# Optimization experiments

Hardware: AMD Instinct MI355X
Metric: run time of the kernel (lower is better)

## Reference

```python
import jax, jax.numpy as jnp
import numpy as np


def _prelu(x, a):
    return jnp.where(x >= 0, x, a * x)


def _conv1x1(x, w, b, a):
    # x: [N,C,H,W], w: [O,C], b: [O] -> PReLU(conv1x1(x))
    y = jnp.einsum('oc,nchw->nohw', w, x) + b[None, :, None, None]
    return _prelu(y, a)


def setup_inputs() -> dict:
    key = jax.random.key(0)
    ks = jax.random.split(key, 8)
    N, C, H, W = 4, 128, 64, 64
    Cr = C // 2  # reduction=2
    sC = 1.0 / np.sqrt(C)
    x = jax.random.normal(ks[0], (N, C, H, W), dtype=jnp.float32)
    w1 = jax.random.normal(ks[1], (Cr, C), dtype=jnp.float32) * sC
    b1 = jnp.zeros((Cr,), dtype=jnp.float32)
    a1 = jnp.asarray(0.25, dtype=jnp.float32)  # PReLU (single shared slope)
    w2 = jax.random.normal(ks[2], (Cr, C), dtype=jnp.float32) * sC
    b2 = jnp.zeros((Cr,), dtype=jnp.float32)
    a2 = jnp.asarray(0.25, dtype=jnp.float32)
    wa = jax.random.normal(ks[3], (C, C), dtype=jnp.float32) * sC
    ba = jnp.zeros((C,), dtype=jnp.float32)
    aa = jnp.asarray(0.25, dtype=jnp.float32)
    return {"x": x, "w1": w1, "b1": b1, "a1": a1,
            "w2": w2, "b2": b2, "a2": a2,
            "wa": wa, "ba": ba, "aa": aa}


def reference(x, w1, b1, a1, w2, b2, a2, wa, ba, aa):
    N, C, H, W = x.shape
    HW = H * W
    e1 = _conv1x1(x, w1, b1, a1).reshape(N, -1, HW)   # [N,Cr,HW]
    e2 = _conv1x1(x, w2, b2, a2).reshape(N, -1, HW)   # [N,Cr,HW]
    asm = _conv1x1(x, wa, ba, aa).reshape(N, C, HW)   # [N,C,HW]
    # ksize=1: per-channel outer products summed over channels == single contraction
    score = jnp.einsum('nci,ncj->nij', e1, e2)        # [N,HW,HW]
    score = jax.nn.softmax(score, axis=2)
    out = jnp.einsum('nij,ncj->nci', score, asm)      # [N,C,HW]
    return out.reshape(N, C, H, W)
```

## Files before the change

### kernel.cpp

```cpp
#include <hip/hip_runtime.h>
#include <hip/hip_bf16.h>
#include <stdint.h>


typedef float   f32x16 __attribute__((ext_vector_type(16)));
typedef __bf16  bf16x8 __attribute__((ext_vector_type(8)));
typedef __bf16  bf16x2 __attribute__((ext_vector_type(2)));
typedef unsigned int u32x4 __attribute__((ext_vector_type(4)));
typedef unsigned int u32x2 __attribute__((ext_vector_type(2)));

#define L2E 1.4426950408889634f
#define NSHIFT (-12.0f * L2E)

#define Q_OFF   (0u)
#define K_OFF   (2u << 20)
#define V_OFF   (4u << 20)
#define DEN_OFF (8u << 20)
#define XTH_OFF ((8u << 20) + (1u << 19))
#define XTL_OFF (XTH_OFF + (4u << 20))
#define WH_OFF  (XTL_OFF + (4u << 20))
#define WL_OFF  (WH_OFF + (1u << 16))
#define OP_OFF  XTH_OFF

__device__ inline unsigned short f2bf(float f) {
  unsigned u = __builtin_bit_cast(unsigned, f);
  return (unsigned short)((u + 0x7FFFu + ((u >> 16) & 1u)) >> 16);
}
__device__ inline float bf2f(unsigned short h) {
  unsigned u = ((unsigned)h) << 16;
  return __builtin_bit_cast(float, u);
}

__device__ inline void gld_lds16(const void* g, void* l) {
  __builtin_amdgcn_global_load_lds(
      (const __attribute__((address_space(1))) unsigned*)g,
      (__attribute__((address_space(3))) unsigned*)l, 16, 0, 0);
}

__global__ __launch_bounds__(256) void transpose_kernel(
    const float* __restrict__ x, char* __restrict__ ws) {
  int bid = blockIdx.x;
  int n = bid >> 7, rem = bid & 127;
  int c0 = (rem >> 6) * 64, s0 = (rem & 63) * 64;
  int tid = threadIdx.x;
  __shared__ float tl[64][65];
  const float* xb = x + (size_t)n * 128 * 4096;
#pragma unroll
  for (int i = 0; i < 16; ++i) {
    int cl = (tid >> 6) * 16 + i;
    tl[cl][tid & 63] = xb[(size_t)(c0 + cl) * 4096 + s0 + (tid & 63)];
  }
  __syncthreads();
  char* XH = ws + XTH_OFF + (size_t)n * (4096 * 256);
  char* XL = ws + XTL_OFF + (size_t)n * (4096 * 256);
#pragma unroll
  for (int it = 0; it < 2; ++it) {
    int sl = (tid >> 3) + it * 32;
    int c8 = (tid & 7) * 8;
    unsigned short uh[8], ul[8];
#pragma unroll
    for (int i = 0; i < 8; ++i) {
      float v = tl[c8 + i][sl];
      unsigned short h = f2bf(v);
      uh[i] = h;
      ul[i] = f2bf(v - bf2f(h));
    }
    u32x4 ph, pl;
    ph.x = ((unsigned)uh[1] << 16) | uh[0]; ph.y = ((unsigned)uh[3] << 16) | uh[2];
    ph.z = ((unsigned)uh[5] << 16) | uh[4]; ph.w = ((unsigned)uh[7] << 16) | uh[6];
    pl.x = ((unsigned)ul[1] << 16) | ul[0]; pl.y = ((unsigned)ul[3] << 16) | ul[2];
    pl.z = ((unsigned)ul[5] << 16) | ul[4]; pl.w = ((unsigned)ul[7] << 16) | ul[6];
    size_t off = (size_t)(s0 + sl) * 256 + c0 * 2 + (tid & 7) * 16;
    *(u32x4*)(XH + off) = ph;
    *(u32x4*)(XL + off) = pl;
  }
}

__global__ void wcast_kernel(const float* __restrict__ w1, const float* __restrict__ w2,
                             const float* __restrict__ wa, char* __restrict__ ws) {
  int idx = blockIdx.x * 256 + threadIdx.x;
  unsigned short* WH = (unsigned short*)(ws + WH_OFF);
  unsigned short* WL = (unsigned short*)(ws + WL_OFF);
#pragma unroll
  for (int r = 0; r < 4; ++r) {
    int i = r * 8192 + idx;
    int oc = i >> 7, c = i & 127;
    float v = oc < 64 ? w1[oc * 128 + c]
            : (oc < 128 ? w2[(oc - 64) * 128 + c] : wa[(oc - 128) * 128 + c]);
    unsigned short h = f2bf(v);
    WH[i] = h;
    WL[i] = f2bf(v - bf2f(h));
  }
}

__global__ __launch_bounds__(256) void conv_kernel(
    char* __restrict__ ws,
    const float* __restrict__ b1, const float* __restrict__ a1,
    const float* __restrict__ b2, const float* __restrict__ a2,
    const float* __restrict__ ba, const float* __restrict__ aa) {
  int bid = blockIdx.x;
  int n = bid >> 7, st = bid & 127;
  int sb = st * 32;
  int tid = threadIdx.x;
  int wid = tid >> 6, lane = tid & 63, l31 = lane & 31, hi = lane >> 5;
  const char* XH = ws + XTH_OFF + (size_t)n * (4096 * 256);
  const char* XL = ws + XTL_OFF + (size_t)n * (4096 * 256);
  const char* WH = ws + WH_OFF;
  const char* WL = ws + WL_OFF;
  int oc0 = wid * 64;

  f32x16 acc[2];
  acc[0] = 0.f; acc[1] = 0.f;
#pragma unroll
  for (int c0 = 0; c0 < 8; ++c0) {
    size_t xo = (size_t)(sb + l31) * 256 + c0 * 32 + hi * 16;
    bf16x8 xh = *(const bf16x8*)(XH + xo);
    bf16x8 xl = *(const bf16x8*)(XL + xo);
#pragma unroll
    for (int mb = 0; mb < 2; ++mb) {
      size_t wo = (size_t)(oc0 + mb * 32 + l31) * 256 + c0 * 32 + hi * 16;
      bf16x8 wh = *(const bf16x8*)(WH + wo);
      bf16x8 wl = *(const bf16x8*)(WL + wo);
      acc[mb] = __builtin_amdgcn_mfma_f32_32x32x16_bf16(wh, xh, acc[mb], 0, 0, 0);
      acc[mb] = __builtin_amdgcn_mfma_f32_32x32x16_bf16(wh, xl, acc[mb], 0, 0, 0);
      acc[mb] = __builtin_amdgcn_mfma_f32_32x32x16_bf16(wl, xh, acc[mb], 0, 0, 0);
    }
  }

  __shared__ float tl[2][64][33];
  char* Qw = ws + Q_OFF + (size_t)n * (4096 * 64 * 2);
  char* Kw = ws + K_OFF + (size_t)n * (4096 * 64 * 2);
  unsigned short* Vw = (unsigned short*)(ws + V_OFF) + (size_t)n * 128 * 4096;

  if (wid < 2) {
    const float* bb = wid ? b2 : b1;
    float slope = wid ? a2[0] : a1[0];
#pragma unroll
    for (int mb = 0; mb < 2; ++mb)
#pragma unroll
      for (int reg = 0; reg < 16; ++reg) {
        int row = mb * 32 + (reg & 3) + 8 * (reg >> 2) + 4 * hi;
        float y = acc[mb][reg] + bb[row];
        y = fmaxf(y, 0.f) + slope * fminf(y, 0.f);
        tl[wid][row][l31] = y;
      }
  } else {
    float slope = aa[0];
#pragma unroll
    for (int mb = 0; mb < 2; ++mb)
#pragma unroll
      for (int reg = 0; reg < 16; ++reg) {
        int dv = (wid - 2) * 64 + mb * 32 + (reg & 3) + 8 * (reg >> 2) + 4 * hi;
        float y = acc[mb][reg] + ba[dv];
        y = fmaxf(y, 0.f) + slope * fminf(y, 0.f);
        Vw[(size_t)dv * 4096 + sb + l31] = f2bf(y);
      }
  }
  __syncthreads();
  if (wid < 2) {
    char* Og = wid ? Kw : Qw;
#pragma unroll
    for (int it = 0; it < 4; ++it) {
      int sl = (lane >> 3) + it * 8;
      unsigned short u[8];
#pragma unroll
      for (int i = 0; i < 8; ++i) u[i] = f2bf(tl[wid][(lane & 7) * 8 + i][sl]);
      u32x4 pv;
      pv.x = ((unsigned)u[1] << 16) | u[0]; pv.y = ((unsigned)u[3] << 16) | u[2];
      pv.z = ((unsigned)u[5] << 16) | u[4]; pv.w = ((unsigned)u[7] << 16) | u[6];
      *(u32x4*)(Og + (size_t)(sb + sl) * 128 + (lane & 7) * 16) = pv;
    }
  }
}

__global__ __launch_bounds__(256, 2) void attn_kernel(char* __restrict__ ws) {
  int bid = blockIdx.x;
  int batch   = (bid >> 1) & 3;
  int quarter = (bid >> 3) & 3;
  int qtile   = ((bid >> 5) << 1) | (bid & 1);
  int tid = threadIdx.x;
  int wid = tid >> 6, lane = tid & 63, l31 = lane & 31, hi = lane >> 5;

  const char* Qb = ws + Q_OFF + (size_t)batch * (4096 * 64 * 2);
  const char* Kb = ws + K_OFF + (size_t)batch * (4096 * 64 * 2);
  const char* Vb = ws + V_OFF + (size_t)batch * (128 * 4096 * 2);

  __shared__ char kbuf[2][64 * 128];
  __shared__ char vbuf[2][128 * 128];

  int q0 = qtile * 128 + wid * 32;

  bf16x8 qf[4];
#pragma unroll
  for (int d0 = 0; d0 < 4; ++d0)
    qf[d0] = *(const bf16x8*)(Qb + (size_t)(q0 + l31) * 128 + d0 * 32 + hi * 16);

  f32x16 oacc[4];
#pragma unroll
  for (int i = 0; i < 4; ++i) oacc[i] = 0.f;
  float den = 0.f;

  int t0 = quarter * 16;

  auto stage = [&](int b, int tile) {
    int kv0 = tile * 64;
#pragma unroll
    for (int i = 0; i < 2; ++i) {
      int base = wid * 2048 + i * 1024;
      int L = base + (lane << 4);
      int r = L >> 7, sl = (L >> 4) & 7;
      const char* src = Kb + (size_t)(kv0 + r) * 128 + ((sl ^ (r & 7)) << 4);
      gld_lds16(src, &kbuf[b][base]);
    }
#pragma unroll
    for (int i = 0; i < 4; ++i) {
      int base = wid * 4096 + i * 1024;
      int L = base + (lane << 4);
      int r = L >> 7, sl = (L >> 4) & 7;
      const char* src = Vb + (size_t)r * 8192 + kv0 * 2 + ((sl ^ (r & 7)) << 4);
      gld_lds16(src, &vbuf[b][base]);
    }
  };

  stage(0, t0);
  __syncthreads();
  int cur = 0;

  for (int t = 0; t < 16; ++t) {
    if (t + 1 < 16) stage(cur ^ 1, t0 + t + 1);

    f32x16 sacc[2];
    sacc[0] = 0.f; sacc[1] = 0.f;
#pragma unroll
    for (int kb = 0; kb < 2; ++kb) {
      int r = kb * 32 + l31;
#pragma unroll
      for (int d0 = 0; d0 < 4; ++d0) {
        bf16x8 kf = *(const bf16x8*)(&kbuf[cur][r * 128 + (((d0 * 2 + hi) ^ (r & 7)) << 4)]);
        sacc[kb] = __builtin_amdgcn_mfma_f32_32x32x16_bf16(kf, qf[d0], sacc[kb], 0, 0, 0);
      }
    }

    float p[2][16];
#pragma unroll
    for (int kb = 0; kb < 2; ++kb)
#pragma unroll
      for (int i = 0; i < 16; ++i) {
        float e = exp2f(fmaf(sacc[kb][i], L2E, NSHIFT));
        p[kb][i] = e;
        den += e;
      }

    unsigned pk[2][8];
#pragma unroll
    for (int kb = 0; kb < 2; ++kb)
#pragma unroll
      for (int m = 0; m < 8; ++m) {
        bf16x2 bp = { (__bf16)p[kb][2 * m], (__bf16)p[kb][2 * m + 1] };
        pk[kb][m] = __builtin_bit_cast(unsigned, bp);
      }

#pragma unroll
    for (int kc = 0; kc < 4; ++kc) {
      const int kb = kc >> 1, bs = (kc & 1) * 4;
      u32x2 r0 = __builtin_amdgcn_permlane32_swap(pk[kb][bs + 0], pk[kb][bs + 2],
                                                  false, false);
      u32x2 r1 = __builtin_amdgcn_permlane32_swap(pk[kb][bs + 1], pk[kb][bs + 3],
                                                  false, false);
      u32x4 pu = {r0.x, r1.x, r0.y, r1.y};
      bf16x8 pf = __builtin_bit_cast(bf16x8, pu);
#pragma unroll
      for (int dvb = 0; dvb < 4; ++dvb) {
        int r = dvb * 32 + l31;
        bf16x8 vf = *(const bf16x8*)(&vbuf[cur][r * 128 + (((kc * 2 + hi) ^ (r & 7)) << 4)]);
        oacc[dvb] = __builtin_amdgcn_mfma_f32_32x32x16_bf16(vf, pf, oacc[dvb], 0, 0, 0);
      }
    }

    __syncthreads();
    cur ^= 1;
  }

  float* OP = (float*)(ws + OP_OFF) +
              (size_t)((batch * 32 + qtile) * 4 + quarter) * 128 * 128;
  int qloc = wid * 32 + l31;
#pragma unroll
  for (int dvb = 0; dvb < 4; ++dvb)
#pragma unroll
    for (int reg = 0; reg < 16; ++reg) {
      int dv = dvb * 32 + (reg & 3) + 8 * (reg >> 2) + 4 * hi;
      OP[dv * 128 + qloc] = oacc[dvb][reg];
    }
  float dtot = den + __shfl_xor(den, 32, 64);
  if (hi == 0) {
    float* DEN = (float*)(ws + DEN_OFF) +
                 (size_t)((batch * 32 + qtile) * 4 + quarter) * 128;
    DEN[qloc] = dtot;
  }
}

__global__ __launch_bounds__(256) void combine_kernel(const char* __restrict__ ws,
                                                      float* __restrict__ out) {
  int idx = blockIdx.x * 256 + threadIdx.x;
  int n = idx >> 19;
  int dv = (idx >> 12) & 127;
  int s = idx & 4095;
  int qt = s >> 7, ql = s & 127;
  const float* OP = (const float*)(ws + OP_OFF);
  const float* DEN = (const float*)(ws + DEN_OFF);
  size_t pb = (size_t)((n * 32 + qt) * 4);
  float num = 0.f, den = 0.f;
#pragma unroll
  for (int h = 0; h < 4; ++h) {
    num += OP[((pb + h) * 128 + dv) * 128 + ql];
    den += DEN[(pb + h) * 128 + ql];
  }
  out[idx] = num / den;
}

extern "C" void kernel_launch(void* const* d_in, const int* in_sizes, int n_in,
                              void* d_out, int out_size, void* d_ws, size_t ws_size,
                              hipStream_t stream) {
  (void)in_sizes; (void)n_in; (void)out_size; (void)ws_size;
  const float* x  = (const float*)d_in[0];
  const float* w1 = (const float*)d_in[1];
  const float* b1 = (const float*)d_in[2];
  const float* a1 = (const float*)d_in[3];
  const float* w2 = (const float*)d_in[4];
  const float* b2 = (const float*)d_in[5];
  const float* a2 = (const float*)d_in[6];
  const float* wa = (const float*)d_in[7];
  const float* ba = (const float*)d_in[8];
  const float* aa = (const float*)d_in[9];
  char* ws = (char*)d_ws;
  float* out = (float*)d_out;

  transpose_kernel<<<dim3(512), dim3(256), 0, stream>>>(x, ws);
  wcast_kernel<<<dim3(32), dim3(256), 0, stream>>>(w1, w2, wa, ws);
  conv_kernel<<<dim3(512), dim3(256), 0, stream>>>(ws, b1, a1, b2, a2, ba, aa);
  attn_kernel<<<dim3(512), dim3(256), 0, stream>>>(ws);
  combine_kernel<<<dim3(8192), dim3(256), 0, stream>>>(ws, out);
}
```

Measured before the change: 73.20 us.

## Double per-wave query rows, split KV eightfold, fold log2e into Q, store bf16 partials

Each wave now handles 64 query rows instead of 32, so every K/V fragment read from LDS feeds twice as many MFMAs. Work is re-split into 16 query tiles of 256 rows times 8 KV splits per batch, keeping the grid size the same. The log2e scale is folded into the Q projection so the inner loop uses a raw exp2 with no fma, and the -12 shift is dropped. Partial outputs are written as bf16 to halve combine traffic. The costs are more registers, eight partials per output instead of four, extra rounding error, and a risk of exp overflow now that the shift is gone.

Result: no change. 74.46 us (+1.7%).

```diff
diff --git a/kernel.cpp b/kernel.cpp
--- a/kernel.cpp
+++ b/kernel.cpp
@@ -10,7 +10,6 @@
 typedef unsigned int u32x2 __attribute__((ext_vector_type(2)));
 
 #define L2E 1.4426950408889634f
-#define NSHIFT (-12.0f * L2E)
 
 #define Q_OFF   (0u)
 #define K_OFF   (2u << 20)
@@ -135,6 +134,7 @@
   if (wid < 2) {
     const float* bb = wid ? b2 : b1;
     float slope = wid ? a2[0] : a1[0];
+    float scl = wid ? 1.0f : L2E;
 #pragma unroll
     for (int mb = 0; mb < 2; ++mb)
 #pragma unroll
@@ -142,7 +142,7 @@
         int row = mb * 32 + (reg & 3) + 8 * (reg >> 2) + 4 * hi;
         float y = acc[mb][reg] + bb[row];
         y = fmaxf(y, 0.f) + slope * fminf(y, 0.f);
-        tl[wid][row][l31] = y;
+        tl[wid][row][l31] = y * scl;
       }
   } else {
     float slope = aa[0];
@@ -175,9 +175,9 @@
 
 __global__ __launch_bounds__(256, 2) void attn_kernel(char* __restrict__ ws) {
   int bid = blockIdx.x;
-  int batch   = (bid >> 1) & 3;
-  int quarter = (bid >> 3) & 3;
-  int qtile   = ((bid >> 5) << 1) | (bid & 1);
+  int qt = bid >> 5;
+  int batch = (bid >> 3) & 3;
+  int split = bid & 7;
   int tid = threadIdx.x;
   int wid = tid >> 6, lane = tid & 63, l31 = lane & 31, hi = lane >> 5;
 
@@ -188,19 +188,24 @@
   __shared__ char kbuf[2][64 * 128];
   __shared__ char vbuf[2][128 * 128];
 
-  int q0 = qtile * 128 + wid * 32;
-
-  bf16x8 qf[4];
-#pragma unroll
-  for (int d0 = 0; d0 < 4; ++d0)
-    qf[d0] = *(const bf16x8*)(Qb + (size_t)(q0 + l31) * 128 + d0 * 32 + hi * 16);
-
-  f32x16 oacc[4];
-#pragma unroll
-  for (int i = 0; i < 4; ++i) oacc[i] = 0.f;
-  float den = 0.f;
-
-  int t0 = quarter * 16;
+  int q0 = qt * 256 + wid * 64;
+
+  bf16x8 qf[2][4];
+#pragma unroll
+  for (int qs = 0; qs < 2; ++qs)
+#pragma unroll
+    for (int d0 = 0; d0 < 4; ++d0)
+      qf[qs][d0] = *(const bf16x8*)(Qb + (size_t)(q0 + qs * 32 + l31) * 128 +
+                                    d0 * 32 + hi * 16);
+
+  f32x16 oacc[2][4];
+#pragma unroll
+  for (int qs = 0; qs < 2; ++qs)
+#pragma unroll
+    for (int i = 0; i < 4; ++i) oacc[qs][i] = 0.f;
+  float den[2] = {0.f, 0.f};
+
+  int t0 = split * 8;
 
   auto stage = [&](int b, int tile) {
     int kv0 = tile * 64;
@@ -226,54 +231,59 @@
   __syncthreads();
   int cur = 0;
 
-  for (int t = 0; t < 16; ++t) {
-    if (t + 1 < 16) stage(cur ^ 1, t0 + t + 1);
-
-    f32x16 sacc[2];
-    sacc[0] = 0.f; sacc[1] = 0.f;
-#pragma unroll
-    for (int kb = 0; kb < 2; ++kb) {
-      int r = kb * 32 + l31;
-#pragma unroll
-      for (int d0 = 0; d0 < 4; ++d0) {
-        bf16x8 kf = *(const bf16x8*)(&kbuf[cur][r * 128 + (((d0 * 2 + hi) ^ (r & 7)) << 4)]);
-        sacc[kb] = __builtin_amdgcn_mfma_f32_32x32x16_bf16(kf, qf[d0], sacc[kb], 0, 0, 0);
-      }
-    }
-
-    float p[2][16];
-#pragma unroll
-    for (int kb = 0; kb < 2; ++kb)
-#pragma unroll
-      for (int i = 0; i < 16; ++i) {
-        float e = exp2f(fmaf(sacc[kb][i], L2E, NSHIFT));
-        p[kb][i] = e;
-        den += e;
-      }
-
-    unsigned pk[2][8];
-#pragma unroll
-    for (int kb = 0; kb < 2; ++kb)
-#pragma unroll
-      for (int m = 0; m < 8; ++m) {
-        bf16x2 bp = { (__bf16)p[kb][2 * m], (__bf16)p[kb][2 * m + 1] };
-        pk[kb][m] = __builtin_bit_cast(unsigned, bp);
-      }
+  for (int t = 0; t < 8; ++t) {
+    if (t + 1 < 8) stage(cur ^ 1, t0 + t + 1);
+
+    unsigned pk[2][2][8];
+#pragma unroll
+    for (int qs = 0; qs < 2; ++qs) {
+      f32x16 sacc[2];
+      sacc[0] = 0.f; sacc[1] = 0.f;
+#pragma unroll
+      for (int kb = 0; kb < 2; ++kb) {
+        int r = kb * 32 + l31;
+#pragma unroll
+        for (int d0 = 0; d0 < 4; ++d0) {
+          bf16x8 kf = *(const bf16x8*)(
+              &kbuf[cur][r * 128 + (((d0 * 2 + hi) ^ (r & 7)) << 4)]);
+          sacc[kb] = __builtin_amdgcn_mfma_f32_32x32x16_bf16(kf, qf[qs][d0],
+                                                             sacc[kb], 0, 0, 0);
+        }
+      }
+#pragma unroll
+      for (int kb = 0; kb < 2; ++kb)
+#pragma unroll
+        for (int m = 0; m < 8; ++m) {
+          float e0 = __builtin_amdgcn_exp2f(sacc[kb][2 * m]);
+          float e1 = __builtin_amdgcn_exp2f(sacc[kb][2 * m + 1]);
+          den[qs] += e0 + e1;
+          bf16x2 bp = { (__bf16)e0, (__bf16)e1 };
+          pk[qs][kb][m] = __builtin_bit_cast(unsigned, bp);
+        }
+    }
 
 #pragma unroll
     for (int kc = 0; kc < 4; ++kc) {
       const int kb = kc >> 1, bs = (kc & 1) * 4;
-      u32x2 r0 = __builtin_amdgcn_permlane32_swap(pk[kb][bs + 0], pk[kb][bs + 2],
-                                                  false, false);
-      u32x2 r1 = __builtin_amdgcn_permlane32_swap(pk[kb][bs + 1], pk[kb][bs + 3],
-                                                  false, false);
-      u32x4 pu = {r0.x, r1.x, r0.y, r1.y};
-      bf16x8 pf = __builtin_bit_cast(bf16x8, pu);
+      bf16x8 pf[2];
+#pragma unroll
+      for (int qs = 0; qs < 2; ++qs) {
+        u32x2 r0 = __builtin_amdgcn_permlane32_swap(pk[qs][kb][bs + 0],
+                                                    pk[qs][kb][bs + 2], false, false);
+        u32x2 r1 = __builtin_amdgcn_permlane32_swap(pk[qs][kb][bs + 1],
+                                                    pk[qs][kb][bs + 3], false, false);
+        u32x4 pu = {r0.x, r1.x, r0.y, r1.y};
+        pf[qs] = __builtin_bit_cast(bf16x8, pu);
+      }
 #pragma unroll
       for (int dvb = 0; dvb < 4; ++dvb) {
         int r = dvb * 32 + l31;
-        bf16x8 vf = *(const bf16x8*)(&vbuf[cur][r * 128 + (((kc * 2 + hi) ^ (r & 7)) << 4)]);
-        oacc[dvb] = __builtin_amdgcn_mfma_f32_32x32x16_bf16(vf, pf, oacc[dvb], 0, 0, 0);
+        bf16x8 vf = *(const bf16x8*)(
+            &vbuf[cur][r * 128 + (((kc * 2 + hi) ^ (r & 7)) << 4)]);
+        oacc[0][dvb] = __builtin_amdgcn_mfma_f32_32x32x16_bf16(vf, pf[0],
+                                                               oacc[0][dvb], 0, 0, 0);
+        oacc[1][dvb] = __builtin_amdgcn_mfma_f32_32x32x16_bf16(vf, pf[1],
+                                                               oacc[1][dvb], 0, 0, 0);
       }
     }
 
@@ -281,21 +291,24 @@
     cur ^= 1;
   }
 
-  float* OP = (float*)(ws + OP_OFF) +
-              (size_t)((batch * 32 + qtile) * 4 + quarter) * 128 * 128;
-  int qloc = wid * 32 + l31;
-#pragma unroll
-  for (int dvb = 0; dvb < 4; ++dvb)
-#pragma unroll
-    for (int reg = 0; reg < 16; ++reg) {
-      int dv = dvb * 32 + (reg & 3) + 8 * (reg >> 2) + 4 * hi;
-      OP[dv * 128 + qloc] = oacc[dvb][reg];
-    }
-  float dtot = den + __shfl_xor(den, 32, 64);
-  if (hi == 0) {
-    float* DEN = (float*)(ws + DEN_OFF) +
-                 (size_t)((batch * 32 + qtile) * 4 + quarter) * 128;
-    DEN[qloc] = dtot;
+  unsigned short* OPu = (unsigned short*)(ws + OP_OFF) +
+                        (size_t)((batch * 16 + qt) * 8 + split) * 128 * 256;
+#pragma unroll
+  for (int qs = 0; qs < 2; ++qs) {
+    int qloc = wid * 64 + qs * 32 + l31;
+#pragma unroll
+    for (int dvb = 0; dvb < 4; ++dvb)
+#pragma unroll
+      for (int reg = 0; reg < 16; ++reg) {
+        int dv = dvb * 32 + (reg & 3) + 8 * (reg >> 2) + 4 * hi;
+        OPu[dv * 256 + qloc] = f2bf(oacc[qs][dvb][reg]);
+      }
+    float dtot = den[qs] + __shfl_xor(den[qs], 32, 64);
+    if (hi == 0) {
+      float* DEN = (float*)(ws + DEN_OFF) +
+                   (size_t)((batch * 16 + qt) * 8 + split) * 256;
+      DEN[qloc] = dtot;
+    }
   }
 }
 
@@ -305,15 +318,15 @@
   int n = idx >> 19;
   int dv = (idx >> 12) & 127;
   int s = idx & 4095;
-  int qt = s >> 7, ql = s & 127;
-  const float* OP = (const float*)(ws + OP_OFF);
+  int qt = s >> 8, ql = s & 255;
+  const unsigned short* OPu = (const unsigned short*)(ws + OP_OFF);
   const float* DEN = (const float*)(ws + DEN_OFF);
-  size_t pb = (size_t)((n * 32 + qt) * 4);
+  size_t pb = (size_t)((n * 16 + qt) * 8);
   float num = 0.f, den = 0.f;
 #pragma unroll
-  for (int h = 0; h < 4; ++h) {
-    num += OP[((pb + h) * 128 + dv) * 128 + ql];
-    den += DEN[(pb + h) * 128 + ql];
+  for (int h = 0; h < 8; ++h) {
+    num += bf2f(OPu[(pb + h) * 128 * 256 + (size_t)dv * 256 + ql]);
+    den += DEN[(pb + h) * 256 + ql];
   }
   out[idx] = num / den;
 }
```
